# Kernel optimization log

Measured on AMD Instinct MI355X. Metric: run time of the kernel, lower is better.

The kernel has to match this reference:

```python
import jax, jax.numpy as jnp
import numpy as np

N = 6144
D_IN = 512
D_OUT = 512
DENSITY = 0.005


def setup_inputs() -> dict:
    key = jax.random.key(0)
    ks = jax.random.split(key, 12)
    x = jax.random.normal(ks[0], (N, D_IN), dtype=jnp.float32)
    adj_a = (jax.random.uniform(ks[1], (N, N)) < DENSITY).astype(jnp.float32)
    adj_b = (jax.random.uniform(ks[2], (N, N)) < DENSITY).astype(jnp.float32)
    # SparseAttention params (xavier-ish scale)
    W_sa = jax.random.normal(ks[3], (D_IN, D_OUT), dtype=jnp.float32) * (1.414 / np.sqrt(D_IN + D_OUT))
    a_sa = jax.random.normal(ks[4], (1, 2 * D_OUT), dtype=jnp.float32) * (1.414 / np.sqrt(1 + 2 * D_OUT))
    # GraphConvolution b params (uniform +-1/sqrt(out))
    stdv = 1.0 / np.sqrt(D_OUT)
    W_gcnb = jax.random.uniform(ks[5], (D_IN, D_OUT), minval=-stdv, maxval=stdv, dtype=jnp.float32)
    b_gcnb = jax.random.uniform(ks[6], (D_OUT,), minval=-stdv, maxval=stdv, dtype=jnp.float32)
    # gate Linear layers: Linear(2*D_IN, 1)
    s = 1.0 / np.sqrt(2 * D_IN)
    Wa = jax.random.uniform(ks[7], (1, 2 * D_IN), minval=-s, maxval=s, dtype=jnp.float32)
    ba = jax.random.uniform(ks[8], (1,), minval=-s, maxval=s, dtype=jnp.float32)
    Wb = jax.random.uniform(ks[9], (1, 2 * D_IN), minval=-s, maxval=s, dtype=jnp.float32)
    bb = jax.random.uniform(ks[10], (1,), minval=-s, maxval=s, dtype=jnp.float32)
    return {"x": x, "adj_a": adj_a, "adj_b": adj_b, "W_sa": W_sa, "a_sa": a_sa,
            "W_gcnb": W_gcnb, "b_gcnb": b_gcnb, "Wa": Wa, "ba": ba, "Wb": Wb, "bb": bb}


def reference(x, adj_a, adj_b, W_sa, a_sa, W_gcnb, b_gcnb, Wa, ba, Wb, bb):
    # type-level gates: sigmoid(Linear(cat[adj@x, x]))
    type_sum_a = adj_a @ x                      # [N, D_IN]
    type_sum_b = adj_b @ x
    attn_a = jax.nn.sigmoid(jnp.concatenate([type_sum_a, x], axis=1) @ Wa.T + ba)  # [N,1]
    attn_b = jax.nn.sigmoid(jnp.concatenate([type_sum_b, x], axis=1) @ Wb.T + bb)

    # SparseAttention over adj_a (edge pattern only)
    h = x @ W_sa                                # [N, D_OUT]
    Hd = h.shape[1]
    s_left = h @ a_sa[0, :Hd]                   # [N] contribution of source node i
    s_right = h @ a_sa[0, Hd:]                  # [N] contribution of target node j
    scores = s_left[:, None] + s_right[None, :]  # [N,N]
    e = jnp.where(adj_a != 0, jnp.exp(-jax.nn.leaky_relu(scores, 0.01)), 0.0)
    attn = e / (jnp.sum(e, axis=1, keepdims=True) + 1e-5)
    x_a = attn @ h                              # [N, D_OUT]

    # GCN branch over adj_b
    x_b = adj_b @ (x @ W_gcnb) + b_gcnb         # [N, D_OUT]

    return jax.nn.sigmoid(attn_a * x_a + attn_b * x_b)
```

## Files before the change

### kernel.cpp

```cpp
#include <hip/hip_runtime.h>
#include <math.h>

#define NN 6144
#define DD 512
#define CAP 128

typedef __bf16 bf16_t;
typedef __bf16 bf16x8 __attribute__((ext_vector_type(8)));
typedef unsigned short u16x8 __attribute__((ext_vector_type(8)));
typedef float f32x4 __attribute__((ext_vector_type(4)));
typedef unsigned u32x4 __attribute__((ext_vector_type(4)));

__device__ __forceinline__ float bf2f(unsigned short u) {
    unsigned v = ((unsigned)u) << 16;
    return __builtin_bit_cast(float, v);
}
__device__ __forceinline__ unsigned short f2bf(float f) {
    unsigned u = __builtin_bit_cast(unsigned, f);
    u += 0x7fffu + ((u >> 16) & 1u);
    return (unsigned short)(u >> 16);
}
__device__ __forceinline__ float sigmoidf_(float z) { return 1.0f / (1.0f + expf(-z)); }

__global__ __launch_bounds__(256) void k_prep(const float* __restrict__ Wsa,
                                              const float* __restrict__ Wg,
                                              const float* __restrict__ a_sa,
                                              unsigned short* __restrict__ wt,
                                              float* __restrict__ wsl, float* __restrict__ wsr) {
    __shared__ float s[64][65];
    int bid = blockIdx.x;
    int wave = threadIdx.x >> 6, lane = threadIdx.x & 63;
    if (bid < 128) {
        int n0 = (bid & 15) * 64;
        int k0 = (bid >> 4) * 64;
        int tx = threadIdx.x & 63, ty = threadIdx.x >> 6;
        const float* src = (n0 < 512) ? Wsa : Wg;
        int nn0 = n0 & 511;
#pragma unroll
        for (int kk = 0; kk < 64; kk += 4)
            s[kk + ty][tx] = src[(size_t)(k0 + kk + ty) * 512 + nn0 + tx];
        __syncthreads();
#pragma unroll
        for (int nn = 0; nn < 64; nn += 4)
            wt[(size_t)(n0 + nn + ty) * 512 + k0 + tx] = f2bf(s[tx][nn + ty]);
    } else {
        int k = (bid - 128) * 4 + wave;
        int n0 = lane * 8;
        const float* wr = Wsa + (size_t)k * 512 + n0;
        float4 w0 = *(const float4*)wr, w1 = *(const float4*)(wr + 4);
        float4 l0 = *(const float4*)(a_sa + n0), l1 = *(const float4*)(a_sa + n0 + 4);
        float4 r0 = *(const float4*)(a_sa + 512 + n0), r1 = *(const float4*)(a_sa + 512 + n0 + 4);
        float sl_ = w0.x*l0.x + w0.y*l0.y + w0.z*l0.z + w0.w*l0.w
                  + w1.x*l1.x + w1.y*l1.y + w1.z*l1.z + w1.w*l1.w;
        float sr_ = w0.x*r0.x + w0.y*r0.y + w0.z*r0.z + w0.w*r0.w
                  + w1.x*r1.x + w1.y*r1.y + w1.z*r1.z + w1.w*r1.w;
#pragma unroll
        for (int off = 32; off; off >>= 1) { sl_ += __shfl_down(sl_, off); sr_ += __shfl_down(sr_, off); }
        if (lane == 0) { wsl[k] = sl_; wsr[k] = sr_; }
    }
}

__global__ __launch_bounds__(256) void k_fused(const float* __restrict__ x,
                                               const bf16_t* __restrict__ wt,
                                               const float* __restrict__ adjA,
                                               const float* __restrict__ adjB,
                                               const float* __restrict__ Wa,
                                               const float* __restrict__ Wb,
                                               const float* __restrict__ wsl,
                                               const float* __restrict__ wsr,
                                               unsigned long long* __restrict__ maskbuf,
                                               unsigned short* __restrict__ h,
                                               unsigned short* __restrict__ g,
                                               float* __restrict__ xal, float* __restrict__ xar,
                                               float* __restrict__ xbl, float* __restrict__ xbr,
                                               float* __restrict__ sl, float* __restrict__ sr) {
    int bid = blockIdx.x;
    int wave = threadIdx.x >> 6, lane = threadIdx.x & 63;
    if (bid < 7680) {
        int grp = bid % 5;
        if (grp < 4) {
            int sid = (bid / 5) * 4 + grp;
            int gw = sid * 4 + wave;
            int row = gw >> 1;
            int half = gw & 1;
            int which = row >= NN;
            int r = which ? row - NN : row;
            const float* adj = which ? adjB : adjA;
            const u32x4* arow = (const u32x4*)(adj + (size_t)r * NN) + half * 768 + lane;
            u32x4 v[12];
#pragma unroll
            for (int j = 0; j < 12; j++) v[j] = arow[j * 64];
            unsigned long long m = 0;
#pragma unroll
            for (int j = 0; j < 12; j++) {
                unsigned long long bits =
                    (unsigned long long)(v[j][0] != 0u) |
                    ((unsigned long long)(v[j][1] != 0u) << 1) |
                    ((unsigned long long)(v[j][2] != 0u) << 2) |
                    ((unsigned long long)(v[j][3] != 0u) << 3);
                m |= bits << (j * 4);
            }
            maskbuf[(size_t)gw * 64 + lane] = m;
        } else {
            int tt = bid / 5;
            int row0 = (tt % (NN / 64)) * 64 + wave * 16;
            int col0 = (tt / (NN / 64)) * 64;
            int lr = lane & 15;
            int kg = (lane >> 4) * 8;

            f32x4 acc[4] = {{0,0,0,0},{0,0,0,0},{0,0,0,0},{0,0,0,0}};
            const float* ap = x + (size_t)(row0 + lr) * DD + kg;
            const bf16_t* bp = wt + (size_t)(col0 + lr) * DD + kg;

            for (int k0 = 0; k0 < DD; k0 += 32) {
                float4 a0 = *(const float4*)(ap + k0);
                float4 a1 = *(const float4*)(ap + k0 + 4);
                u16x8 au;
                au[0] = f2bf(a0.x); au[1] = f2bf(a0.y); au[2] = f2bf(a0.z); au[3] = f2bf(a0.w);
                au[4] = f2bf(a1.x); au[5] = f2bf(a1.y); au[6] = f2bf(a1.z); au[7] = f2bf(a1.w);
                bf16x8 a = __builtin_bit_cast(bf16x8, au);
#pragma unroll
                for (int n = 0; n < 4; n++) {
                    bf16x8 b = *(const bf16x8*)(bp + (size_t)n * 16 * DD + k0);
                    acc[n] = __builtin_amdgcn_mfma_f32_16x16x32_bf16(a, b, acc[n], 0, 0, 0);
                }
            }
            int dcol = lane & 15;
            int dr0 = (lane >> 4) * 4;
#pragma unroll
            for (int n = 0; n < 4; n++) {
                int col = col0 + n * 16 + dcol;
                unsigned short* dst = (col < 512) ? h : g;
                int cc = col & 511;
#pragma unroll
                for (int rr = 0; rr < 4; rr++) {
                    int mr = row0 + dr0 + rr;
                    dst[(size_t)mr * 512 + cc] = f2bf(acc[n][rr]);
                }
            }
        }
    } else {
        int pid = bid - 7680;
        int row = pid * 4 + wave;
        int k0 = lane * 8;
        const float* xr_ = x + (size_t)row * DD + k0;
        float4 v0 = *(const float4*)xr_;
        float4 v1 = *(const float4*)(xr_ + 4);
        float xv[8] = {v0.x, v0.y, v0.z, v0.w, v1.x, v1.y, v1.z, v1.w};
        float d[6] = {0, 0, 0, 0, 0, 0};
        const float* srcs[6] = {Wa + k0, Wa + 512 + k0, Wb + k0, Wb + 512 + k0, wsl + k0, wsr + k0};
#pragma unroll
        for (int q = 0; q < 6; q++) {
            float4 w0 = *(const float4*)srcs[q];
            float4 w1 = *(const float4*)(srcs[q] + 4);
            float wv[8] = {w0.x, w0.y, w0.z, w0.w, w1.x, w1.y, w1.z, w1.w};
#pragma unroll
            for (int j = 0; j < 8; j++) d[q] += xv[j] * wv[j];
        }
#pragma unroll
        for (int off = 32; off; off >>= 1)
#pragma unroll
            for (int q = 0; q < 6; q++) d[q] += __shfl_down(d[q], off);
        if (lane == 0) {
            xal[row] = d[0]; xar[row] = d[1];
            xbl[row] = d[2]; xbr[row] = d[3];
            sl[row] = d[4]; sr[row] = d[5];
        }
    }
}

__global__ __launch_bounds__(256) void k_final(
    const unsigned long long* __restrict__ maskbuf,
    const unsigned short* __restrict__ h, const unsigned short* __restrict__ g,
    const float* __restrict__ sl, const float* __restrict__ sr,
    const float* __restrict__ xal, const float* __restrict__ xar,
    const float* __restrict__ xbl, const float* __restrict__ xbr,
    const float* __restrict__ ba, const float* __restrict__ bb,
    const float* __restrict__ bias, float* __restrict__ out) {
    int i = blockIdx.x;
    int tid = threadIdx.x;
    int wave = tid >> 6, lane = tid & 63;
    __shared__ float w[CAP];
    __shared__ int ja[CAP], jb[CAP];
    __shared__ int tot[4];
    __shared__ float s_denom, s_ga, s_gb;

    int half = wave & 1;
    int gw = (wave < 2) ? (i * 2 + half) : ((NN + i) * 2 + half);
    unsigned long long m = maskbuf[(size_t)gw * 64 + lane];
    int c = __popcll(m);
    int p = c;
#pragma unroll
    for (int off = 1; off < 64; off <<= 1) {
        int t = __shfl_up(p, off);
        if (lane >= off) p += t;
    }
    if (lane == 63) tot[wave] = p;
    __syncthreads();
    int base = (wave == 1) ? tot[0] : (wave == 3) ? tot[2] : 0;
    int pos = base + p - c;
    int* dst = (wave < 2) ? ja : jb;
    while (m) {
        int b = __ffsll((long long)m) - 1;
        m &= m - 1;
        int col = half * 3072 + (((b >> 2) * 64 + lane) << 2) + (b & 3);
        if (pos < CAP) dst[pos] = col;
        pos++;
    }
    __syncthreads();
    int cA = tot[0] + tot[1]; cA = cA > CAP ? CAP : cA;
    int cB = tot[2] + tot[3]; cB = cB > CAP ? CAP : cB;

    if (tid < cA) {
        int j = ja[tid];
        float s = sl[i] + sr[j];
        float lrelu = s > 0.f ? s : 0.01f * s;
        w[tid] = expf(-lrelu);
    }
    __syncthreads();

    if (tid < 64) {
        float p2 = 0.f, gasum = 0.f, gbsum = 0.f;
        for (int t = tid; t < cA; t += 64) { p2 += w[t]; gasum += xal[ja[t]]; }
        for (int t = tid; t < cB; t += 64) gbsum += xbl[jb[t]];
#pragma unroll
        for (int off = 32; off; off >>= 1) {
            p2 += __shfl_down(p2, off);
            gasum += __shfl_down(gasum, off);
            gbsum += __shfl_down(gbsum, off);
        }
        if (tid == 0) {
            s_denom = p2;
            s_ga = sigmoidf_(gasum + xar[i] + ba[0]);
            s_gb = sigmoidf_(gbsum + xbr[i] + bb[0]);
        }
    }
    __syncthreads();
    float inv = 1.f / (s_denom + 1e-5f);
    float ga = s_ga, gb = s_gb;

    int d0 = tid * 2;
    float a0 = 0, a1 = 0, b0 = 0, b1 = 0;
#pragma unroll 4
    for (int t = 0; t < cA; t++) {
        unsigned hv = *(const unsigned*)(h + (size_t)ja[t] * 512 + d0);
        float wt_ = w[t];
        a0 += wt_ * bf2f((unsigned short)(hv & 0xffff));
        a1 += wt_ * bf2f((unsigned short)(hv >> 16));
    }
#pragma unroll 4
    for (int t = 0; t < cB; t++) {
        unsigned gv = *(const unsigned*)(g + (size_t)jb[t] * 512 + d0);
        b0 += bf2f((unsigned short)(gv & 0xffff));
        b1 += bf2f((unsigned short)(gv >> 16));
    }
    float z0 = ga * (a0 * inv) + gb * (b0 + bias[d0]);
    float z1 = ga * (a1 * inv) + gb * (b1 + bias[d0 + 1]);
    out[(size_t)i * 512 + d0]     = sigmoidf_(z0);
    out[(size_t)i * 512 + d0 + 1] = sigmoidf_(z1);
}

extern "C" void kernel_launch(void* const* d_in, const int* in_sizes, int n_in,
                              void* d_out, int out_size, void* d_ws, size_t ws_size,
                              hipStream_t stream) {
    const float* x    = (const float*)d_in[0];
    const float* adjA = (const float*)d_in[1];
    const float* adjB = (const float*)d_in[2];
    const float* Wsa  = (const float*)d_in[3];
    const float* a_sa = (const float*)d_in[4];
    const float* Wg   = (const float*)d_in[5];
    const float* bg   = (const float*)d_in[6];
    const float* Wa   = (const float*)d_in[7];
    const float* ba   = (const float*)d_in[8];
    const float* Wb   = (const float*)d_in[9];
    const float* bb   = (const float*)d_in[10];
    float* out = (float*)d_out;

    char* ws = (char*)d_ws;
    size_t off = 0;
    auto alloc = [&](size_t bytes) -> void* {
        void* p = ws + off;
        off += (bytes + 255) & ~(size_t)255;
        return p;
    };
    unsigned short* wt = (unsigned short*)alloc((size_t)1024 * DD * 2);
    unsigned short* h  = (unsigned short*)alloc((size_t)NN * DD * 2);
    unsigned short* g  = (unsigned short*)alloc((size_t)NN * DD * 2);
    unsigned long long* maskbuf = (unsigned long long*)alloc((size_t)24576 * 64 * 8);
    float* xal = (float*)alloc((size_t)NN * 4);
    float* xar = (float*)alloc((size_t)NN * 4);
    float* xbl = (float*)alloc((size_t)NN * 4);
    float* xbr = (float*)alloc((size_t)NN * 4);
    float* sl  = (float*)alloc((size_t)NN * 4);
    float* sr  = (float*)alloc((size_t)NN * 4);
    float* wsl = (float*)alloc((size_t)DD * 4);
    float* wsr = (float*)alloc((size_t)DD * 4);

    k_prep<<<256, 256, 0, stream>>>(Wsa, Wg, a_sa, wt, wsl, wsr);
    k_fused<<<9216, 256, 0, stream>>>(x, (const bf16_t*)wt, adjA, adjB, Wa, Wb, wsl, wsr,
                                      maskbuf, h, g, xal, xar, xbl, xbr, sl, sr);
    k_final<<<NN, 256, 0, stream>>>(maskbuf, h, g, sl, sr, xal, xar, xbl, xbr,
                                    ba, bb, bg, out);
}
```

Measured before the change: 172.3 us.

## Build adjacency bitmask with wave ballots over a grid-strided flat scan

The adjacency-to-bitmask scan now has each thread read one 16-byte chunk per iteration from a flat grid-strided index over both matrices. Per-lane bit packing is replaced by wave-wide __ballot calls, and a few lanes write the mask words, which changes the mask layout. The final kernel's decode of column indices is updated to match the new layout, and only 48 lanes per wave load mask words. The aim is to shorten load latency chains and register pressure per thread (12 vector loads in flight before) so the streaming read of the 300MB of adjacency data runs closer to bandwidth. The cost is more ballot instructions and some branch divergence.

After: 176.8 us. 1.03x slower.

```diff
diff --git a/kernel.cpp b/kernel.cpp
--- a/kernel.cpp
+++ b/kernel.cpp
@@ -4,6 +4,8 @@
 #define NN 6144
 #define DD 512
 #define CAP 128
+#define SCAN_T (6144 * 256)
+#define HALF_U4 (NN * (NN / 4))
 
 typedef __bf16 bf16_t;
 typedef __bf16 bf16x8 __attribute__((ext_vector_type(8)));
@@ -68,7 +70,7 @@
                                                const float* __restrict__ Wb,
                                                const float* __restrict__ wsl,
                                                const float* __restrict__ wsr,
-                                               unsigned long long* __restrict__ maskbuf,
+                                               unsigned long long* __restrict__ maskw,
                                                unsigned short* __restrict__ h,
                                                unsigned short* __restrict__ g,
                                                float* __restrict__ xal, float* __restrict__ xar,
@@ -79,28 +81,28 @@
     if (bid < 7680) {
         int grp = bid % 5;
         if (grp < 4) {
-            int sid = (bid / 5) * 4 + grp;
-            int gw = sid * 4 + wave;
-            int row = gw >> 1;
-            int half = gw & 1;
-            int which = row >= NN;
-            int r = which ? row - NN : row;
-            const float* adj = which ? adjB : adjA;
-            const u32x4* arow = (const u32x4*)(adj + (size_t)r * NN) + half * 768 + lane;
-            u32x4 v[12];
-#pragma unroll
-            for (int j = 0; j < 12; j++) v[j] = arow[j * 64];
-            unsigned long long m = 0;
+            int sblk = (bid / 5) * 4 + grp;
+            int gt = sblk * 256 + threadIdx.x;
+            int wb0 = gt - lane;
+            const u32x4* a4 = (const u32x4*)adjA;
+            const u32x4* b4 = (const u32x4*)adjB;
 #pragma unroll
             for (int j = 0; j < 12; j++) {
-                unsigned long long bits =
-                    (unsigned long long)(v[j][0] != 0u) |
-                    ((unsigned long long)(v[j][1] != 0u) << 1) |
-                    ((unsigned long long)(v[j][2] != 0u) << 2) |
-                    ((unsigned long long)(v[j][3] != 0u) << 3);
-                m |= bits << (j * 4);
+                int f = gt + j * SCAN_T;
+                u32x4 v;
+                if (f < HALF_U4) v = a4[f];
+                else             v = b4[f - HALF_U4];
+                unsigned long long b0 = __ballot(v[0] != 0u);
+                unsigned long long b1 = __ballot(v[1] != 0u);
+                unsigned long long b2 = __ballot(v[2] != 0u);
+                unsigned long long b3 = __ballot(v[3] != 0u);
+                int seg = (wb0 + j * SCAN_T) >> 6;
+                if (lane < 4) {
+                    unsigned long long bb = (lane == 0) ? b0 : (lane == 1) ? b1
+                                          : (lane == 2) ? b2 : b3;
+                    maskw[(size_t)seg * 4 + lane] = bb;
+                }
             }
-            maskbuf[(size_t)gw * 64 + lane] = m;
         } else {
             int tt = bid / 5;
             int row0 = (tt % (NN / 64)) * 64 + wave * 16;
@@ -170,7 +172,7 @@
 }
 
 __global__ __launch_bounds__(256) void k_final(
-    const unsigned long long* __restrict__ maskbuf,
+    const unsigned long long* __restrict__ maskw,
     const unsigned short* __restrict__ h, const unsigned short* __restrict__ g,
     const float* __restrict__ sl, const float* __restrict__ sr,
     const float* __restrict__ xal, const float* __restrict__ xar,
@@ -185,9 +187,10 @@
     __shared__ int tot[4];
     __shared__ float s_denom, s_ga, s_gb;
 
-    int half = wave & 1;
-    int gw = (wave < 2) ? (i * 2 + half) : ((NN + i) * 2 + half);
-    unsigned long long m = maskbuf[(size_t)gw * 64 + lane];
+    int whalf = wave & 1;
+    size_t rowbase = (size_t)((wave < 2) ? i : (NN + i)) * 96;
+    int widx = whalf * 48 + lane;
+    unsigned long long m = (lane < 48) ? maskw[rowbase + widx] : 0ull;
     int c = __popcll(m);
     int p = c;
 #pragma unroll
@@ -203,7 +206,7 @@
     while (m) {
         int b = __ffsll((long long)m) - 1;
         m &= m - 1;
-        int col = half * 3072 + (((b >> 2) * 64 + lane) << 2) + (b & 3);
+        int col = (widx >> 2) * 256 + b * 4 + (widx & 3);
         if (pos < CAP) dst[pos] = col;
         pos++;
     }
@@ -286,7 +289,7 @@
     unsigned short* wt = (unsigned short*)alloc((size_t)1024 * DD * 2);
     unsigned short* h  = (unsigned short*)alloc((size_t)NN * DD * 2);
     unsigned short* g  = (unsigned short*)alloc((size_t)NN * DD * 2);
-    unsigned long long* maskbuf = (unsigned long long*)alloc((size_t)24576 * 64 * 8);
+    unsigned long long* maskw = (unsigned long long*)alloc((size_t)294912 * 4 * 8);
     float* xal = (float*)alloc((size_t)NN * 4);
     float* xar = (float*)alloc((size_t)NN * 4);
     float* xbl = (float*)alloc((size_t)NN * 4);
@@ -298,7 +301,7 @@
 
     k_prep<<<256, 256, 0, stream>>>(Wsa, Wg, a_sa, wt, wsl, wsr);
     k_fused<<<9216, 256, 0, stream>>>(x, (const bf16_t*)wt, adjA, adjB, Wa, Wb, wsl, wsr,
-                                      maskbuf, h, g, xal, xar, xbl, xbr, sl, sr);
-    k_final<<<NN, 256, 0, stream>>>(maskbuf, h, g, sl, sr, xal, xar, xbl, xbr,
+                                      maskw, h, g, xal, xar, xbl, xbr, sl, sr);
+    k_final<<<NN, 256, 0, stream>>>(maskw, h, g, sl, sr, xal, xar, xbl, xbr,
                                     ba, bb, bg, out);
 }
```
